# Performance work log

Measured on AMD Instinct MI355X. Metric: run time of the kernel, lower is better.

The kernel has to match this reference:

```python
import jax, jax.numpy as jnp
import numpy as np

HID = 1024   # hidden_dim
H = 16       # num_head
D = 64       # head_dim
W = 64       # window_size (one-sided attention radius)


def setup_inputs() -> dict:
    key = jax.random.key(0)
    ks = jax.random.split(key, 10)
    B, S = 2, 4096
    s = 0.02
    X = jax.random.normal(ks[0], (B, S, HID), jnp.float32)
    mask = jnp.ones((B, S), jnp.float32)
    Wq = jax.random.normal(ks[1], (HID, H * D), jnp.float32) * s
    bq = jnp.zeros((H * D,), jnp.float32)
    Wk = jax.random.normal(ks[2], (HID, H * D), jnp.float32) * s
    bk = jnp.zeros((H * D,), jnp.float32)
    Wv = jax.random.normal(ks[3], (HID, H * D), jnp.float32) * s
    bv = jnp.zeros((H * D,), jnp.float32)
    Wo = jax.random.normal(ks[4], (H * D, HID), jnp.float32) * s
    bo = jnp.zeros((HID,), jnp.float32)
    return dict(X=X, mask=mask, Wq=Wq, bq=bq, Wk=Wk, bk=bk, Wv=Wv, bv=bv, Wo=Wo, bo=bo)


def _chunk3(T, nC):
    # T: [B,H,S,D] -> [B,H,nC,3W,D]: for chunk c, keys of chunks c-1, c, c+1 (zero-padded at ends)
    B, Hh, S, Dd = T.shape
    Tp = jnp.pad(T, ((0, 0), (0, 0), (W, W), (0, 0))).reshape(B, Hh, nC + 2, W, Dd)
    return jnp.concatenate([Tp[:, :, :-2], Tp[:, :, 1:-1], Tp[:, :, 2:]], axis=3)


def reference(X, mask, Wq, bq, Wk, bk, Wv, bv, Wo, bo):
    B, S0, _ = X.shape
    pad = W - S0 % W  # matches torch: always >= 1 (full window if divisible)
    Xp = jnp.pad(X, ((0, 0), (0, pad), (0, 0)))
    mp = jnp.pad(mask, ((0, 0), (0, pad)))  # padded keys masked out
    S = S0 + pad
    nC = S // W

    def proj(Wm, b):
        return (Xp @ Wm + b).reshape(B, S, H, D).transpose(0, 2, 1, 3)  # [B,H,S,D]

    Q, K, V = proj(Wq, bq), proj(Wk, bk), proj(Wv, bv)
    Qc = Q.reshape(B, H, nC, W, D)
    K3 = _chunk3(K, nC)
    V3 = _chunk3(V, nC)

    # banded scores: query i attends keys j with |i - j| <= W
    scores = jnp.einsum('bhcqd,bhckd->bhcqk', Qc, K3) / jnp.asarray(np.sqrt(D), jnp.float32)
    qi = jnp.arange(W)[:, None]
    kj = jnp.arange(3 * W)[None, :]
    band = (kj >= qi) & (kj <= qi + 2 * W)  # [W, 3W]
    m3 = jnp.pad(mp, ((0, 0), (W, W))).reshape(B, nC + 2, W)
    m3 = jnp.concatenate([m3[:, :-2], m3[:, 1:-1], m3[:, 2:]], axis=2)  # [B,nC,3W]
    valid = band[None, None, None, :, :] & (m3[:, None, :, None, :] > 0)
    scores = jnp.where(valid, scores, -1e9)
    A = jax.nn.softmax(scores, axis=-1)
    ctx = jnp.einsum('bhcqk,bhckd->bhcqd', A, V3).reshape(B, H, S, D)
    out = ctx.transpose(0, 2, 1, 3).reshape(B, S, H * D) @ Wo + bo
    return out[:, :S0]
```

## Files before the change

### kernel.cpp

```cpp
#include <hip/hip_runtime.h>

typedef unsigned short u16;
typedef unsigned int u32;
typedef __bf16 bf16x8 __attribute__((ext_vector_type(8)));
typedef u16 u16x8 __attribute__((ext_vector_type(8)));
typedef float floatx4 __attribute__((ext_vector_type(4)));

#define MFMA16(a, b, c) __builtin_amdgcn_mfma_f32_16x16x32_bf16((a), (b), (c), 0, 0, 0)

#define B_ 2
#define S0 4096
#define NH 16
#define HD 64
#define HID 1024
#define VS 280
#define PS 200

__device__ __forceinline__ float bf2f(u16 u) {
  union { u32 i; float f; } x; x.i = ((u32)u) << 16; return x.f;
}
__device__ __forceinline__ u16 f2bf(float f) {
  union { float f; u32 i; } x; x.f = f;
  u32 r = x.i + 0x7FFFu + ((x.i >> 16) & 1u);
  return (u16)(r >> 16);
}

__device__ __forceinline__ void glds16(const u16* g, u16* l) {
  __builtin_amdgcn_global_load_lds(
      (const __attribute__((address_space(1))) u32*)g,
      (__attribute__((address_space(3))) u32*)l, 16, 0, 0);
}

__global__ __launch_bounds__(256) void prep(
    const float* __restrict__ X, const float* __restrict__ mask,
    const float* __restrict__ Wq, const float* __restrict__ bq,
    const float* __restrict__ Wk, const float* __restrict__ bk,
    const float* __restrict__ Wv, const float* __restrict__ bv,
    const float* __restrict__ Wo, const float* __restrict__ bo,
    u16* __restrict__ cX, u16* __restrict__ cmask, u16* __restrict__ cb,
    u16* __restrict__ WqkvT, u16* __restrict__ WoT) {
  __shared__ u16 tile[64][66];
  int bid = blockIdx.x;
  if (bid < 4096) {
    int i = (bid * 256 + threadIdx.x) * 8;
    const float4* Xv = (const float4*)(X + i);
    float4 a = Xv[0], b = Xv[1];
    u16x8 v;
    v[0] = f2bf(a.x); v[1] = f2bf(a.y); v[2] = f2bf(a.z); v[3] = f2bf(a.w);
    v[4] = f2bf(b.x); v[5] = f2bf(b.y); v[6] = f2bf(b.z); v[7] = f2bf(b.w);
    *(u16x8*)(cX + i) = v;
  } else if (bid < 4144) {
    int tid = (bid - 4096) * 256 + threadIdx.x;
    if (tid < B_ * S0) {
      cmask[tid] = f2bf(mask[tid]);
    } else {
      int j = tid - B_ * S0;
      int seg = j >> 10, idx = j & 1023;
      const float* src = (seg == 0) ? bq : (seg == 1) ? bk : (seg == 2) ? bv : bo;
      cb[seg * 1024 + idx] = f2bf(src[idx]);
    }
  } else {
    int idx = bid - 4144;
    int mat = idx >> 8;
    const float* src = (mat == 0) ? Wq : (mat == 1) ? Wk : (mat == 2) ? Wv : Wo;
    u16* dst = (mat < 3) ? (WqkvT + (size_t)mat * HID * HID) : WoT;
    int t0 = ((idx >> 4) & 15) * 64;
    int c0 = (idx & 15) * 64;
    int tx = threadIdx.x & 63, ty = threadIdx.x >> 6;
#pragma unroll
    for (int i = 0; i < 16; i++) {
      int r = i * 4 + ty;
      tile[r][tx] = f2bf(src[(size_t)(t0 + r) * HID + c0 + tx]);
    }
    __syncthreads();
#pragma unroll
    for (int i = 0; i < 16; i++) {
      int r = i * 4 + ty;
      dst[(size_t)(c0 + r) * HID + t0 + tx] = tile[tx][r];
    }
  }
}

template <int BN, int MODE, int NMAJOR, int SWZ>
__global__ __launch_bounds__(256) void gemm_bf16_tn(
    const u16* __restrict__ A, const u16* __restrict__ Bt,
    const u16* __restrict__ cb, void* __restrict__ outp, int K) {
  constexpr int NT = BN / 32;
  __shared__ alignas(16) u16 sA[128 * 64];
  __shared__ alignas(16) u16 sB[BN * 64];
  int t = threadIdx.x;
  int wave = t >> 6, lane = t & 63;
  int wm = wave >> 1, wn = wave & 1;
  int quad = lane >> 4, l16 = lane & 15;
  int tile_m, tile_n;
  if (SWZ) {
    int lin = blockIdx.y * gridDim.x + blockIdx.x;
    int wg = (lin & 7) * 256 + (lin >> 3);
    tile_m = (wg >> 5) * 128;
    tile_n = (wg & 31) * BN;
  } else {
    tile_m = (NMAJOR ? blockIdx.y : blockIdx.x) * 128;
    tile_n = (NMAJOR ? blockIdx.x : blockIdx.y) * BN;
  }

  floatx4 acc[4][NT] = {};

  int row_l = lane >> 3;
  int col_l = ((lane & 7) ^ row_l) * 8;
  const u16* Ag = A + (size_t)(tile_m + wave * 8 + row_l) * K + col_l;
  const u16* Bg = Bt + (size_t)(tile_n + wave * 8 + row_l) * K + col_l;
  u16* lA = sA + wave * 8 * 64;
  u16* lB = sB + wave * 8 * 64;

  for (int k0 = 0; k0 < K; k0 += 64) {
    __syncthreads();
#pragma unroll
    for (int r = 0; r < 4; r++)
      glds16(Ag + (size_t)(r * 32) * K + k0, lA + r * 2048);
#pragma unroll
    for (int r = 0; r < BN / 32; r++)
      glds16(Bg + (size_t)(r * 32) * K + k0, lB + r * 2048);
    __syncthreads();

#pragma unroll
    for (int ks = 0; ks < 2; ks++) {
      bf16x8 af[4], bfr[NT];
#pragma unroll
      for (int mt = 0; mt < 4; mt++) {
        int row = wm * 64 + mt * 16 + l16;
        int p = (ks * 4 + quad) ^ (row & 7);
        af[mt] = *(const bf16x8*)(sA + row * 64 + p * 8);
      }
#pragma unroll
      for (int nt = 0; nt < NT; nt++) {
        int row = wn * (BN / 2) + nt * 16 + l16;
        int p = (ks * 4 + quad) ^ (row & 7);
        bfr[nt] = *(const bf16x8*)(sB + row * 64 + p * 8);
      }
#pragma unroll
      for (int mt = 0; mt < 4; mt++)
#pragma unroll
        for (int nt = 0; nt < NT; nt++)
          acc[mt][nt] = MFMA16(af[mt], bfr[nt], acc[mt][nt]);
    }
  }

  if (MODE == 0) {
    u16* op = (u16*)outp;
#pragma unroll
    for (int mt = 0; mt < 4; mt++) {
      int row0 = tile_m + wm * 64 + mt * 16 + quad * 4;
      int bb = row0 >> 12;
      int sbase = row0 & (S0 - 1);
#pragma unroll
      for (int nt = 0; nt < NT; nt++) {
        int col = tile_n + wn * (BN / 2) + nt * 16 + l16;
        int p = col >> 10;
        int rem = col & 1023;
        float bias = bf2f(cb[p * 1024 + rem]);
        int hh = rem >> 6, dd = rem & 63;
        u16* dp = op + ((size_t)(((p * 2 + bb) * NH + hh)) * S0 + sbase) * HD + dd;
#pragma unroll
        for (int r = 0; r < 4; r++)
          dp[(size_t)r * HD] = f2bf(acc[mt][nt][r] + bias);
      }
    }
  } else {
    float* op = (float*)outp;
#pragma unroll
    for (int mt = 0; mt < 4; mt++) {
      int row0 = tile_m + wm * 64 + mt * 16 + quad * 4;
#pragma unroll
      for (int nt = 0; nt < NT; nt++) {
        int col = tile_n + wn * (BN / 2) + nt * 16 + l16;
        float bias = bf2f(cb[3 * 1024 + col]);
        float* dp = op + (size_t)row0 * HID + col;
#pragma unroll
        for (int r = 0; r < 4; r++)
          dp[(size_t)r * HID] = acc[mt][nt][r] + bias;
      }
    }
  }
}

__global__ __launch_bounds__(256) void attn_win2(
    const u16* __restrict__ Q, const u16* __restrict__ Kp,
    const u16* __restrict__ Vp, const u16* __restrict__ cmask,
    u16* __restrict__ ctx) {
  __shared__ alignas(16) u16 buf0[64 * VS];
  __shared__ alignas(16) u16 sP[4 * 16 * PS];
  __shared__ u16 sMk[256];

  int bid = blockIdx.x;
  int cc = bid & 31, h = (bid >> 5) & 15, b = bid >> 9;
  int c0 = cc * 2;
  int t = threadIdx.x;
  int wave = t >> 6, lane = t & 63;
  int quad = lane >> 4, l16 = lane & 15;
  int koff = wave * 16;

  const u16* Qb = Q + (size_t)(b * NH + h) * S0 * HD;
  const u16* Kb = Kp + (size_t)(b * NH + h) * S0 * HD;
  const u16* Vb = Vp + (size_t)(b * NH + h) * S0 * HD;
  int kbase = (c0 - 1) * 64;

  int rrow = lane >> 3;
  int csrc = ((lane & 7) ^ rrow) * 8;
#pragma unroll
  for (int p = 0; p < 8; p++) {
    int sl0 = p * 32 + wave * 8;
    int key = kbase + sl0 + rrow;
    int kc = key < 0 ? 0 : (key > S0 - 1 ? S0 - 1 : key);
    glds16(Kb + (size_t)kc * HD + csrc, buf0 + sl0 * 64);
  }
  {
    int j = kbase + t;
    sMk[t] = (j >= 0 && j < S0) ? cmask[(size_t)b * S0 + j] : (u16)0;
  }
  __syncthreads();

  floatx4 sc[9] = {};
  int qrowA = c0 * 64 + wave * 16 + l16;
#pragma unroll
  for (int ks = 0; ks < 2; ks++) {
    bf16x8 aq = *(const bf16x8*)(Qb + (size_t)qrowA * HD + ks * 32 + quad * 8);
#pragma unroll
    for (int nt = 0; nt < 9; nt++) {
      int slot = koff + nt * 16 + l16;
      int pch = ((ks * 4 + quad) ^ (l16 & 7)) * 8;
      bf16x8 bk = *(const bf16x8*)(buf0 + slot * 64 + pch);
      sc[nt] = MFMA16(aq, bk, sc[nt]);
    }
  }

  u16x8 vreg[9];
#pragma unroll
  for (int i = 0; i < 9; i++) {
    int e = i * 256 + t;
    if (e < 2176) {
      int dg = e / 272;
      int slot = e - dg * 272;
      int key = kbase + slot;
      int kc = key < 0 ? 0 : (key > S0 - 1 ? S0 - 1 : key);
      vreg[i] = *(const u16x8*)(Vb + (size_t)kc * HD + dg * 8);
    }
  }

  u16* myP = sP + wave * 16 * PS;

#define SOFTMAX_P(off)                                                       \
  do {                                                                       \
    float kmask[9];                                                          \
    _Pragma("unroll") for (int nt = 0; nt < 9; nt++)                         \
        kmask[nt] = bf2f(sMk[(off) + koff + nt * 16 + l16]);                 \
    _Pragma("unroll") for (int reg = 0; reg < 4; reg++) {                    \
      int qrel = (off) + wave * 16 + quad * 4 + reg;                         \
      float v[9];                                                            \
      float m = -3e38f;                                                      \
      _Pragma("unroll") for (int nt = 0; nt < 9; nt++) {                     \
        int slot = (off) + koff + nt * 16 + l16;                             \
        bool ok = (slot >= qrel) && (slot <= qrel + 128) && (kmask[nt] > 0.f); \
        float s = ok ? sc[nt][reg] * 0.125f : -1e30f;                        \
        v[nt] = s;                                                           \
        m = fmaxf(m, s);                                                     \
      }                                                                      \
      _Pragma("unroll") for (int o2 = 1; o2 <= 8; o2 <<= 1)                  \
          m = fmaxf(m, __shfl_xor(m, o2));                                   \
      float sum = 0.f;                                                       \
      _Pragma("unroll") for (int nt = 0; nt < 9; nt++) {                     \
        float pp = __expf(v[nt] - m);                                        \
        v[nt] = pp;                                                          \
        sum += pp;                                                           \
      }                                                                      \
      _Pragma("unroll") for (int o2 = 1; o2 <= 8; o2 <<= 1)                  \
          sum += __shfl_xor(sum, o2);                                        \
      float inv = 1.0f / sum;                                                \
      int prow = (quad * 4 + reg) * PS;                                      \
      _Pragma("unroll") for (int nt = 0; nt < 9; nt++)                       \
          myP[prow + nt * 16 + l16] = f2bf(v[nt] * inv);                     \
      myP[prow + 144 + l16] = 0;                                             \
    }                                                                        \
  } while (0)

#define PV_CTX(off)                                                          \
  do {                                                                       \
    floatx4 oc[4] = {};                                                      \
    _Pragma("unroll") for (int ks = 0; ks < 5; ks++) {                       \
      bf16x8 ap = *(const bf16x8*)(myP + l16 * PS + ks * 32 + quad * 8);     \
      _Pragma("unroll") for (int nt = 0; nt < 4; nt++) {                     \
        bf16x8 bv = *(const bf16x8*)(buf0 + (nt * 16 + l16) * VS + (off) +   \
                                     koff + ks * 32 + quad * 8);             \
        oc[nt] = MFMA16(ap, bv, oc[nt]);                                     \
      }                                                                      \
    }                                                                        \
    int srow = c0 * 64 + (off) + wave * 16 + quad * 4;                       \
    _Pragma("unroll") for (int nt = 0; nt < 4; nt++) {                       \
      u16* dp = ctx + (size_t)(b * S0 + srow) * HID + h * HD + nt * 16 + l16; \
      _Pragma("unroll") for (int reg = 0; reg < 4; reg++)                    \
          dp[(size_t)reg * HID] = f2bf(oc[nt][reg]);                         \
    }                                                                        \
  } while (0)

  SOFTMAX_P(0);

#pragma unroll
  for (int nt = 0; nt < 9; nt++) sc[nt] = (floatx4){0.f, 0.f, 0.f, 0.f};
  int qrowB = qrowA + 64;
#pragma unroll
  for (int ks = 0; ks < 2; ks++) {
    bf16x8 aq = *(const bf16x8*)(Qb + (size_t)qrowB * HD + ks * 32 + quad * 8);
#pragma unroll
    for (int nt = 0; nt < 9; nt++) {
      int slot = 64 + koff + nt * 16 + l16;
      int pch = ((ks * 4 + quad) ^ (l16 & 7)) * 8;
      bf16x8 bk = *(const bf16x8*)(buf0 + slot * 64 + pch);
      sc[nt] = MFMA16(aq, bk, sc[nt]);
    }
  }
  __syncthreads();

#pragma unroll
  for (int i = 0; i < 9; i++) {
    int e = i * 256 + t;
    if (e < 2176) {
      int dg = e / 272;
      int slot = e - dg * 272;
#pragma unroll
      for (int j = 0; j < 8; j++) buf0[(dg * 8 + j) * VS + slot] = vreg[i][j];
    }
  }
  __syncthreads();

  PV_CTX(0);
  SOFTMAX_P(64);
  PV_CTX(64);
#undef SOFTMAX_P
#undef PV_CTX
}

extern "C" void kernel_launch(void* const* d_in, const int* in_sizes, int n_in,
                              void* d_out, int out_size, void* d_ws, size_t ws_size,
                              hipStream_t stream) {
  const float* X = (const float*)d_in[0];
  const float* mask = (const float*)d_in[1];
  const float* Wq = (const float*)d_in[2];
  const float* bq = (const float*)d_in[3];
  const float* Wk = (const float*)d_in[4];
  const float* bk = (const float*)d_in[5];
  const float* Wv = (const float*)d_in[6];
  const float* bv = (const float*)d_in[7];
  const float* Wo = (const float*)d_in[8];
  const float* bo = (const float*)d_in[9];
  char* ws = (char*)d_ws;

  const size_t MB = 1048576;
  u16* cmask = (u16*)(ws + 256);
  u16* cb = (u16*)(ws + 256 + 16384);
  u16* cX = (u16*)(ws + 1 * MB);
  u16* WqkvT = (u16*)(ws + 17 * MB);
  u16* WoT = (u16*)(ws + 23 * MB);
  u16* QKV = (u16*)(ws + 25 * MB);
  u16* CTX = cX;

  const size_t per_qkv = (size_t)B_ * NH * S0 * HD;

  prep<<<4096 + 48 + 1024, 256, 0, stream>>>(X, mask, Wq, bq, Wk, bk, Wv, bv,
                                             Wo, bo, cX, cmask, cb, WqkvT, WoT);
  gemm_bf16_tn<96, 0, 1, 1><<<dim3(32, 64), 256, 0, stream>>>(cX, WqkvT, cb, QKV, HID);
  attn_win2<<<dim3(B_ * NH * 32), 256, 0, stream>>>(QKV, QKV + per_qkv,
                                                    QKV + 2 * per_qkv, cmask, CTX);
  gemm_bf16_tn<128, 1, 0, 0><<<dim3(64, 8), 256, 0, stream>>>(CTX, WoT, cb, d_out, HID);
}
```

Baseline: 220.3 us.

## Double-buffer GEMM LDS tiles with async prefetch and explicit vmcnt waits

Converts the bf16 GEMM main loop to a two-stage LDS ping-pong. The next K tile is issued via global_load_lds before computing on the current one, and explicit s_waitcnt vmcnt counts wait only for the current tile. This aims to hide global-load latency behind MFMA work. It doubles LDS per block, which may lower occupancy, and splits the template into two kernels with fixed shared buffers.

```diff
diff --git a/kernel.cpp b/kernel.cpp
--- a/kernel.cpp
+++ b/kernel.cpp
@@ -29,6 +29,13 @@
   __builtin_amdgcn_global_load_lds(
       (const __attribute__((address_space(1))) u32*)g,
       (__attribute__((address_space(3))) u32*)l, 16, 0, 0);
+}
+
+template <int N>
+__device__ __forceinline__ void waitvm() {
+  if constexpr (N == 0) asm volatile("s_waitcnt vmcnt(0)" ::: "memory");
+  else if constexpr (N == 7) asm volatile("s_waitcnt vmcnt(7)" ::: "memory");
+  else if constexpr (N == 8) asm volatile("s_waitcnt vmcnt(8)" ::: "memory");
 }
 
 __global__ __launch_bounds__(256) void prep(
@@ -81,13 +88,13 @@
   }
 }
 
-template <int BN, int MODE, int NMAJOR, int SWZ>
-__global__ __launch_bounds__(256) void gemm_bf16_tn(
+template <int BN, int MODE, int SWZ>
+__device__ __forceinline__ void gemm_body(
     const u16* __restrict__ A, const u16* __restrict__ Bt,
-    const u16* __restrict__ cb, void* __restrict__ outp, int K) {
+    const u16* __restrict__ cb, void* __restrict__ outp, int K,
+    u16 (*__restrict__ sA)[128 * 64], u16 (*__restrict__ sB)[BN * 64]) {
   constexpr int NT = BN / 32;
-  __shared__ alignas(16) u16 sA[128 * 64];
-  __shared__ alignas(16) u16 sB[BN * 64];
+  constexpr int NCALLS = 4 + BN / 32;
   int t = threadIdx.x;
   int wave = t >> 6, lane = t & 63;
   int wm = wave >> 1, wn = wave & 1;
@@ -99,8 +106,8 @@
     tile_m = (wg >> 5) * 128;
     tile_n = (wg & 31) * BN;
   } else {
-    tile_m = (NMAJOR ? blockIdx.y : blockIdx.x) * 128;
-    tile_n = (NMAJOR ? blockIdx.x : blockIdx.y) * BN;
+    tile_m = blockIdx.x * 128;
+    tile_n = blockIdx.y * BN;
   }
 
   floatx4 acc[4][NT] = {};
@@ -109,19 +116,32 @@
   int col_l = ((lane & 7) ^ row_l) * 8;
   const u16* Ag = A + (size_t)(tile_m + wave * 8 + row_l) * K + col_l;
   const u16* Bg = Bt + (size_t)(tile_n + wave * 8 + row_l) * K + col_l;
-  u16* lA = sA + wave * 8 * 64;
-  u16* lB = sB + wave * 8 * 64;
-
-  for (int k0 = 0; k0 < K; k0 += 64) {
-    __syncthreads();
-#pragma unroll
-    for (int r = 0; r < 4; r++)
-      glds16(Ag + (size_t)(r * 32) * K + k0, lA + r * 2048);
-#pragma unroll
-    for (int r = 0; r < BN / 32; r++)
-      glds16(Bg + (size_t)(r * 32) * K + k0, lB + r * 2048);
-    __syncthreads();
-
+  const int lofs = wave * 8 * 64;
+  const int NTILES = K >> 6;
+
+#define STAGE_T(TT)                                                        \
+  do {                                                                     \
+    int k0_ = (TT) * 64;                                                   \
+    u16* lA_ = &sA[(TT) & 1][lofs];                                        \
+    u16* lB_ = &sB[(TT) & 1][lofs];                                        \
+    _Pragma("unroll") for (int r = 0; r < 4; r++)                          \
+        glds16(Ag + (size_t)(r * 32) * K + k0_, lA_ + r * 2048);           \
+    _Pragma("unroll") for (int r = 0; r < BN / 32; r++)                    \
+        glds16(Bg + (size_t)(r * 32) * K + k0_, lB_ + r * 2048);           \
+  } while (0)
+
+  STAGE_T(0);
+  for (int T = 0; T < NTILES; ++T) {
+    if (T < NTILES - 1) {
+      STAGE_T(T + 1);
+      waitvm<NCALLS>();
+    } else {
+      waitvm<0>();
+    }
+    __builtin_amdgcn_s_barrier();
+    __builtin_amdgcn_sched_barrier(0);
+
+    int bi = T & 1;
 #pragma unroll
     for (int ks = 0; ks < 2; ks++) {
       bf16x8 af[4], bfr[NT];
@@ -129,13 +149,13 @@
       for (int mt = 0; mt < 4; mt++) {
         int row = wm * 64 + mt * 16 + l16;
         int p = (ks * 4 + quad) ^ (row & 7);
-        af[mt] = *(const bf16x8*)(sA + row * 64 + p * 8);
+        af[mt] = *(const bf16x8*)(&sA[bi][row * 64 + p * 8]);
       }
 #pragma unroll
       for (int nt = 0; nt < NT; nt++) {
         int row = wn * (BN / 2) + nt * 16 + l16;
         int p = (ks * 4 + quad) ^ (row & 7);
-        bfr[nt] = *(const bf16x8*)(sB + row * 64 + p * 8);
+        bfr[nt] = *(const bf16x8*)(&sB[bi][row * 64 + p * 8]);
       }
 #pragma unroll
       for (int mt = 0; mt < 4; mt++)
@@ -143,7 +163,10 @@
         for (int nt = 0; nt < NT; nt++)
           acc[mt][nt] = MFMA16(af[mt], bfr[nt], acc[mt][nt]);
     }
-  }
+    __builtin_amdgcn_sched_barrier(0);
+    __builtin_amdgcn_s_barrier();
+  }
+#undef STAGE_T
 
   if (MODE == 0) {
     u16* op = (u16*)outp;
@@ -181,6 +204,22 @@
       }
     }
   }
+}
+
+__global__ __launch_bounds__(256) void gemm_qkv(
+    const u16* __restrict__ A, const u16* __restrict__ Bt,
+    const u16* __restrict__ cb, void* __restrict__ outp, int K) {
+  __shared__ alignas(16) u16 sA[2][128 * 64];
+  __shared__ alignas(16) u16 sB[2][96 * 64];
+  gemm_body<96, 0, 1>(A, Bt, cb, outp, K, sA, sB);
+}
+
+__global__ __launch_bounds__(256) void gemm_out(
+    const u16* __restrict__ A, const u16* __restrict__ Bt,
+    const u16* __restrict__ cb, void* __restrict__ outp, int K) {
+  __shared__ alignas(16) u16 sA[2][128 * 64];
+  __shared__ alignas(16) u16 sB[2][128 * 64];
+  gemm_body<128, 1, 0>(A, Bt, cb, outp, K, sA, sB);
 }
 
 __global__ __launch_bounds__(256) void attn_win2(
@@ -366,8 +405,8 @@
 
   prep<<<4096 + 48 + 1024, 256, 0, stream>>>(X, mask, Wq, bq, Wk, bk, Wv, bv,
                                              Wo, bo, cX, cmask, cb, WqkvT, WoT);
-  gemm_bf16_tn<96, 0, 1, 1><<<dim3(32, 64), 256, 0, stream>>>(cX, WqkvT, cb, QKV, HID);
+  gemm_qkv<<<dim3(32, 64), 256, 0, stream>>>(cX, WqkvT, cb, QKV, HID);
   attn_win2<<<dim3(B_ * NH * 32), 256, 0, stream>>>(QKV, QKV + per_qkv,
                                                     QKV + 2 * per_qkv, cmask, CTX);
-  gemm_bf16_tn<128, 1, 0, 0><<<dim3(64, 8), 256, 0, stream>>>(CTX, WoT, cb, d_out, HID);
-}
+  gemm_out<<<dim3(64, 8), 256, 0, stream>>>(CTX, WoT, cb, d_out, HID);
+}
```

After: 224.5 us. About the same (+1.9%).

## Split QKV projection GEMM into three row-range launches

Applied to the files above, without the earlier changes.

The QKV projection GEMM is split into three launches, each covering a range of M tiles via a new mbase offset, and the swizzle is generalised to the grid size. The gemm template becomes a device body wrapped by two concrete kernels. The likely aim is to shrink each launch's working set or change wave scheduling, at the cost of extra launch overhead and per-launch tail effects.

```diff
diff --git a/kernel.cpp b/kernel.cpp
--- a/kernel.cpp
+++ b/kernel.cpp
@@ -81,10 +81,10 @@
   }
 }
 
-template <int BN, int MODE, int NMAJOR, int SWZ>
-__global__ __launch_bounds__(256) void gemm_bf16_tn(
+template <int BN, int MODE, int SWZ>
+__device__ __forceinline__ void gemm_body(
     const u16* __restrict__ A, const u16* __restrict__ Bt,
-    const u16* __restrict__ cb, void* __restrict__ outp, int K) {
+    const u16* __restrict__ cb, void* __restrict__ outp, int K, int mbase) {
   constexpr int NT = BN / 32;
   __shared__ alignas(16) u16 sA[128 * 64];
   __shared__ alignas(16) u16 sB[BN * 64];
@@ -95,12 +95,14 @@
   int tile_m, tile_n;
   if (SWZ) {
     int lin = blockIdx.y * gridDim.x + blockIdx.x;
-    int wg = (lin & 7) * 256 + (lin >> 3);
-    tile_m = (wg >> 5) * 128;
+    int nwg = gridDim.x * gridDim.y;
+    int cpx = nwg >> 3;
+    int wg = (lin & 7) * cpx + (lin >> 3);
+    tile_m = (mbase + (wg >> 5)) * 128;
     tile_n = (wg & 31) * BN;
   } else {
-    tile_m = (NMAJOR ? blockIdx.y : blockIdx.x) * 128;
-    tile_n = (NMAJOR ? blockIdx.x : blockIdx.y) * BN;
+    tile_m = (mbase + blockIdx.x) * 128;
+    tile_n = blockIdx.y * BN;
   }
 
   floatx4 acc[4][NT] = {};
@@ -181,6 +183,18 @@
       }
     }
   }
+}
+
+__global__ __launch_bounds__(256) void gemm_qkv(
+    const u16* __restrict__ A, const u16* __restrict__ Bt,
+    const u16* __restrict__ cb, void* __restrict__ outp, int K, int mbase) {
+  gemm_body<96, 0, 1>(A, Bt, cb, outp, K, mbase);
+}
+
+__global__ __launch_bounds__(256) void gemm_out(
+    const u16* __restrict__ A, const u16* __restrict__ Bt,
+    const u16* __restrict__ cb, void* __restrict__ outp, int K, int mbase) {
+  gemm_body<128, 1, 0>(A, Bt, cb, outp, K, mbase);
 }
 
 __global__ __launch_bounds__(256) void attn_win2(
@@ -366,8 +380,10 @@
 
   prep<<<4096 + 48 + 1024, 256, 0, stream>>>(X, mask, Wq, bq, Wk, bk, Wv, bv,
                                              Wo, bo, cX, cmask, cb, WqkvT, WoT);
-  gemm_bf16_tn<96, 0, 1, 1><<<dim3(32, 64), 256, 0, stream>>>(cX, WqkvT, cb, QKV, HID);
+  gemm_qkv<<<dim3(32, 22), 256, 0, stream>>>(cX, WqkvT, cb, QKV, HID, 0);
+  gemm_qkv<<<dim3(32, 22), 256, 0, stream>>>(cX, WqkvT, cb, QKV, HID, 22);
+  gemm_qkv<<<dim3(32, 20), 256, 0, stream>>>(cX, WqkvT, cb, QKV, HID, 44);
   attn_win2<<<dim3(B_ * NH * 32), 256, 0, stream>>>(QKV, QKV + per_qkv,
                                                     QKV + 2 * per_qkv, cmask, CTX);
-  gemm_bf16_tn<128, 1, 0, 0><<<dim3(64, 8), 256, 0, stream>>>(CTX, WoT, cb, d_out, HID);
-}
+  gemm_out<<<dim3(64, 8), 256, 0, stream>>>(CTX, WoT, cb, d_out, HID, 0);
+}
```

Result: slower. 225.7 us (+2.5%).
